# Optimization experiments

Hardware: AMD Instinct MI355X
Metric: run time of the kernel (lower is better)

The kernel has to match this reference:

```python
import jax, jax.numpy as jnp
import numpy as np

N_NODES = 100000
N_EDGES = 600000
D = 128          # model_dim
R = 50           # deprel_size


def setup_inputs() -> dict:
    key = jax.random.key(0)
    ks = jax.random.split(key, 20)
    s = 1.0 / np.sqrt(D)
    inp = jax.random.normal(ks[0], (N_NODES, D), dtype=jnp.float32)
    deprel_edge = jax.random.randint(ks[1], (N_EDGES,), 0, R)
    deparc_edge = jax.random.randint(ks[2], (N_EDGES,), 0, 4)
    edge_index = jax.random.randint(ks[3], (2, N_EDGES), 0, N_NODES)
    # parameters (nn.Linear weights stored as [out, in]; gates are Linear(D,1))
    V_in = jax.random.normal(ks[4], (D, D), dtype=jnp.float32) * s
    V_out = jax.random.normal(ks[5], (D, D), dtype=jnp.float32) * s
    W_self = jax.random.normal(ks[6], (D, D), dtype=jnp.float32) * s
    W_norel = jax.random.normal(ks[7], (D, D), dtype=jnp.float32) * s
    V_in_gate = jax.random.normal(ks[8], (1, D), dtype=jnp.float32) * s
    V_out_gate = jax.random.normal(ks[9], (1, D), dtype=jnp.float32) * s
    W_self_gate = jax.random.normal(ks[10], (1, D), dtype=jnp.float32) * s
    W_norel_gate = jax.random.normal(ks[11], (1, D), dtype=jnp.float32) * s
    b_in = jax.random.normal(ks[12], (R, D), dtype=jnp.float32) * 0.02
    b_out = jax.random.normal(ks[13], (R, D), dtype=jnp.float32) * 0.02
    b_in_gate = jax.random.normal(ks[14], (R, 1), dtype=jnp.float32) * 0.02 + 1.0
    b_out_gate = jax.random.normal(ks[15], (R, 1), dtype=jnp.float32) * 0.02 + 1.0
    return {
        "inp": inp, "deprel_edge": deprel_edge, "deparc_edge": deparc_edge,
        "edge_index": edge_index,
        "V_in": V_in, "b_in": b_in, "V_in_gate": V_in_gate, "b_in_gate": b_in_gate,
        "V_out": V_out, "b_out": b_out, "V_out_gate": V_out_gate, "b_out_gate": b_out_gate,
        "W_self": W_self, "W_self_gate": W_self_gate,
        "W_norel": W_norel, "W_norel_gate": W_norel_gate,
    }


def reference(inp, deprel_edge, deparc_edge, edge_index,
              V_in, b_in, V_in_gate, b_in_gate,
              V_out, b_out, V_out_gate, b_out_gate,
              W_self, W_self_gate, W_norel, W_norel_gate):
    # deparc type codes: 0=align(in), 1=opposite(out), 2=self, 3=norelation
    num_nodes = inp.shape[0]
    src, tgt = edge_index[0], edge_index[1]
    # transformed node features per edge type: [4, N, D]
    T = jnp.stack([inp @ V_in.T, inp @ V_out.T, inp @ W_self.T, inp @ W_norel.T])
    # gate pre-activations per edge type: [4, N, 1]
    G = jnp.stack([inp @ V_in_gate.T, inp @ V_out_gate.T,
                   inp @ W_self_gate.T, inp @ W_norel_gate.T])
    zeros_b = jnp.zeros_like(b_in)
    zeros_bg = jnp.zeros_like(b_in_gate)
    B = jnp.stack([b_in, b_out, zeros_b, zeros_b])        # [4, R, D] (self/norel have no relation bias)
    Bg = jnp.stack([b_in_gate, b_out_gate, zeros_bg, zeros_bg])  # [4, R, 1]
    # per-edge gather + relation bias
    msg = T[deparc_edge, src] + B[deparc_edge, deprel_edge]        # [E, D]
    gate = jax.nn.sigmoid(G[deparc_edge, src] + Bg[deparc_edge, deprel_edge])  # [E, 1]
    # scatter-add to target nodes
    return jax.ops.segment_sum(msg * gate, tgt, num_segments=num_nodes)
```

## Files before the change

### kernel.cpp

```cpp
#include <hip/hip_runtime.h>
#include <hip/hip_bf16.h>

#define D 128

typedef __bf16 bf16x8 __attribute__((ext_vector_type(8)));
typedef __bf16 bf16x4 __attribute__((ext_vector_type(4)));
typedef __bf16 bf16x2 __attribute__((ext_vector_type(2)));
typedef float  f32x4  __attribute__((ext_vector_type(4)));
typedef float  f32x2  __attribute__((ext_vector_type(2)));
typedef unsigned int u32x4 __attribute__((ext_vector_type(4)));

template <int ISBF>
__device__ __forceinline__ bf16x8 ld8(const void* p, size_t elem)
{
    if (ISBF) return *(const bf16x8*)((const __bf16*)p + elem);
    const f32x4* f = (const f32x4*)((const float*)p + elem);
    f32x4 lo = f[0], hi = f[1];
    bf16x8 r;
    r[0] = (__bf16)lo[0]; r[1] = (__bf16)lo[1]; r[2] = (__bf16)lo[2]; r[3] = (__bf16)lo[3];
    r[4] = (__bf16)hi[0]; r[5] = (__bf16)hi[1]; r[6] = (__bf16)hi[2]; r[7] = (__bf16)hi[3];
    return r;
}
template <int ISBF>
__device__ __forceinline__ float ldf(const void* p, size_t elem)
{
    return ISBF ? (float)((const __bf16*)p)[elem] : ((const float*)p)[elem];
}

__device__ __forceinline__ f32x2 bfpair(unsigned int u)
{
    f32x2 r;
    r[0] = __builtin_bit_cast(float, u << 16);
    r[1] = __builtin_bit_cast(float, u & 0xffff0000u);
    return r;
}

__device__ __forceinline__ f32x2 pkfma(f32x2 a, f32x2 b, f32x2 c)
{
    f32x2 d;
    asm("v_pk_fma_f32 %0, %1, %2, %3" : "=v"(d) : "v"(a), "v"(b), "v"(c));
    return d;
}

__global__ __launch_bounds__(256) void hist_detect_kernel(
    const int* __restrict__ tgt, int* __restrict__ counts, int E,
    const unsigned int* __restrict__ w, int* __restrict__ flag)
{
    __shared__ int cnt[256];
    int e = blockIdx.x * 256 + threadIdx.x;
    if (e < E) atomicAdd(&counts[tgt[e]], 1);
    if (blockIdx.x == 0) {
        int c = 0;
#pragma unroll
        for (int i = 0; i < 4; ++i) {
            unsigned int v = w[threadIdx.x * 4 + i];
            unsigned int ex = (v >> 7) & 0xFF;
            if (ex >= 90 && ex <= 134) ++c;
        }
        cnt[threadIdx.x] = c;
        __syncthreads();
        for (int s = 128; s > 0; s >>= 1) {
            if (threadIdx.x < s) cnt[threadIdx.x] += cnt[threadIdx.x + s];
            __syncthreads();
        }
        if (threadIdx.x == 0) flag[0] = (cnt[0] > 614) ? 1 : 0;
    }
}

template <int ISBF>
__device__ __forceinline__ void gate_bias_body(
    const void* __restrict__ A,
    const void* __restrict__ g0, const void* __restrict__ g1,
    const void* __restrict__ g2, const void* __restrict__ g3,
    const void* __restrict__ b_in, const void* __restrict__ b_out,
    const void* __restrict__ bg_in, const void* __restrict__ bg_out,
    float* __restrict__ G, __bf16* __restrict__ Bz, float* __restrict__ Bgz,
    int M)
{
    if (blockIdx.x < 101 && threadIdx.x < 128) {
        int row = blockIdx.x;
        int tid = threadIdx.x;
        float v = 0.f, gv = 0.f;
        if (row < 50) {
            v  = ldf<ISBF>(b_in, (size_t)row * D + tid);
            gv = ldf<ISBF>(bg_in, row);
        } else if (row < 100) {
            int rr = row - 50;
            v  = ldf<ISBF>(b_out, (size_t)rr * D + tid);
            gv = ldf<ISBF>(bg_out, rr);
        }
        Bz[(size_t)row * D + tid] = (__bf16)v;
        if (tid == 0) Bgz[row] = gv;
    }

    int node = blockIdx.x * 16 + (threadIdx.x >> 4);
    if (node >= M) return;
    int lane16 = threadIdx.x & 15;
    int dd = lane16 * 8;
    bf16x8 a  = ld8<ISBF>(A, (size_t)node * D + dd);
    bf16x8 q0 = ld8<ISBF>(g0, dd);
    bf16x8 q1 = ld8<ISBF>(g1, dd);
    bf16x8 q2 = ld8<ISBF>(g2, dd);
    bf16x8 q3 = ld8<ISBF>(g3, dd);
    float s0 = 0.f, s1 = 0.f, s2 = 0.f, s3 = 0.f;
#pragma unroll
    for (int k = 0; k < 8; ++k) {
        float af = (float)a[k];
        s0 = fmaf(af, (float)q0[k], s0);
        s1 = fmaf(af, (float)q1[k], s1);
        s2 = fmaf(af, (float)q2[k], s2);
        s3 = fmaf(af, (float)q3[k], s3);
    }
#pragma unroll
    for (int off = 8; off > 0; off >>= 1) {
        s0 += __shfl_xor(s0, off);
        s1 += __shfl_xor(s1, off);
        s2 += __shfl_xor(s2, off);
        s3 += __shfl_xor(s3, off);
    }
    if (lane16 == 0) {
        G[(size_t)0 * M + node] = s0;
        G[(size_t)1 * M + node] = s1;
        G[(size_t)2 * M + node] = s2;
        G[(size_t)3 * M + node] = s3;
    }
}

__global__ __launch_bounds__(256) void gate_bias_kernel(
    const void* __restrict__ A,
    const void* __restrict__ g0, const void* __restrict__ g1,
    const void* __restrict__ g2, const void* __restrict__ g3,
    const void* __restrict__ b_in, const void* __restrict__ b_out,
    const void* __restrict__ bg_in, const void* __restrict__ bg_out,
    float* __restrict__ G, __bf16* __restrict__ Bz, float* __restrict__ Bgz,
    int M, const int* __restrict__ flag)
{
    if (flag[0]) gate_bias_body<1>(A, g0, g1, g2, g3, b_in, b_out, bg_in, bg_out, G, Bz, Bgz, M);
    else         gate_bias_body<0>(A, g0, g1, g2, g3, b_in, b_out, bg_in, bg_out, G, Bz, Bgz, M);
}

__global__ __launch_bounds__(256) void scan1_kernel(
    const int* __restrict__ counts, int* __restrict__ rowptr,
    int* __restrict__ bsum, int M)
{
    __shared__ int sh[256];
    int base = blockIdx.x * 1024 + threadIdx.x * 4;
    int v[4];
#pragma unroll
    for (int k = 0; k < 4; ++k)
        v[k] = (base + k < M) ? counts[base + k] : 0;
    int tot = v[0] + v[1] + v[2] + v[3];
    sh[threadIdx.x] = tot;
    __syncthreads();
    for (int off = 1; off < 256; off <<= 1) {
        int t = (threadIdx.x >= off) ? sh[threadIdx.x - off] : 0;
        __syncthreads();
        sh[threadIdx.x] += t;
        __syncthreads();
    }
    int run = sh[threadIdx.x] - tot;
#pragma unroll
    for (int k = 0; k < 4; ++k) {
        if (base + k < M) rowptr[base + k] = run;
        run += v[k];
    }
    if (threadIdx.x == 255) bsum[blockIdx.x] = sh[255];
}

__global__ __launch_bounds__(256) void scan3_kernel(
    int* __restrict__ rowptr, int* __restrict__ cursor,
    const int* __restrict__ bsum, int M, int E)
{
    int b = blockIdx.x;
    int o = 0;
    for (int i = 0; i < b; ++i) o += bsum[i];
    int base = b * 1024 + threadIdx.x * 4;
#pragma unroll
    for (int k = 0; k < 4; ++k) {
        int i = base + k;
        if (i < M) {
            int r = rowptr[i] + o;
            rowptr[i] = r;
            cursor[i] = r;
        }
    }
    if (b == 0 && threadIdx.x == 0) rowptr[M] = E;
}

__global__ __launch_bounds__(256) void scatter_kernel(
    const int* __restrict__ deprel, const int* __restrict__ deparc,
    const int* __restrict__ src, const int* __restrict__ tgt,
    int* __restrict__ cursor, int2* __restrict__ recs, int E)
{
    int e = blockIdx.x * 256 + threadIdx.x;
    if (e >= E) return;
    int g = tgt[e];
    int pos = atomicAdd(&cursor[g], 1);
    recs[pos] = make_int2(src[e], (deprel[e] << 2) | deparc[e]);
}

template <int ISBF>
__device__ __forceinline__ void edge_agg_body(
    const void* __restrict__ inp, const float* __restrict__ G,
    const __bf16* __restrict__ Bz, const float* __restrict__ Bgz,
    const int* __restrict__ rowptr, const int2* __restrict__ recs,
    __bf16* __restrict__ AG, __bf16* __restrict__ BA, int M)
{
    const int g = blockIdx.x * 16 + (threadIdx.x >> 4);
    if (g >= M) return;
    const int lane16 = threadIdx.x & 15;
    const int dd = lane16 * 8;

    const int beg = rowptr[g], end = rowptr[g + 1];
    const int n = end - beg;

    f32x2 a0[4], a1[4], a2[4], a3[4], ba[4];
#pragma unroll
    for (int k = 0; k < 4; ++k) {
        a0[k] = (f32x2){0.f, 0.f}; a1[k] = (f32x2){0.f, 0.f};
        a2[k] = (f32x2){0.f, 0.f}; a3[k] = (f32x2){0.f, 0.f};
        ba[k] = (f32x2){0.f, 0.f};
    }

    bf16x8 v0 = {}, bz0 = {}, v1 = {}, bz1 = {};
    float gp0 = 0.f, bg0 = 0.f, gp1 = 0.f, bg1 = 0.f;
    int t0 = 0, t1 = 0;
    int2 r2 = make_int2(0, 0);

    auto issue = [&](int2 rec, bf16x8& v, bf16x8& bz, float& gp, float& bg, int& t) {
        t = rec.y & 3;
        int r = rec.y >> 2;
        int bidx = (t < 2) ? t * 50 + r : 100;
        gp = G[(size_t)t * M + rec.x];
        bg = Bgz[bidx];
        v  = ld8<ISBF>(inp, (size_t)rec.x * D + dd);
        bz = *(const bf16x8*)(Bz + (size_t)bidx * D + dd);
    };

    if (n > 0) issue(recs[beg], v0, bz0, gp0, bg0, t0);
    if (n > 1) issue(recs[beg + 1], v1, bz1, gp1, bg1, t1);
    if (n > 2) r2 = recs[beg + 2];

    for (int e = 0; e < n; ++e) {
        const bf16x8 v = v0, bz = bz0;
        const float gp = gp0, bg = bg0;
        const int t = t0;

        v0 = v1; bz0 = bz1; gp0 = gp1; bg0 = bg1; t0 = t1;
        if (e + 2 < n) {
            issue(r2, v1, bz1, gp1, bg1, t1);
            if (e + 3 < n) r2 = recs[beg + e + 3];
        }

        const float gate = 1.f / (1.f + __expf(-(gp + bg)));
        const float w0s = (t == 0) ? gate : 0.f;
        const float w1s = (t == 1) ? gate : 0.f;
        const float w2s = (t == 2) ? gate : 0.f;
        const float w3s = (t == 3) ? gate : 0.f;
        const f32x2 w0 = {w0s, w0s}, w1 = {w1s, w1s};
        const f32x2 w2 = {w2s, w2s}, w3 = {w3s, w3s};
        const f32x2 gg = {gate, gate};

        const u32x4 uv = __builtin_bit_cast(u32x4, v);
        const u32x4 ub = __builtin_bit_cast(u32x4, bz);
#pragma unroll
        for (int k = 0; k < 4; ++k) {
            const f32x2 vf = bfpair(uv[k]);
            const f32x2 bf = bfpair(ub[k]);
            a0[k] = pkfma(vf, w0, a0[k]);
            a1[k] = pkfma(vf, w1, a1[k]);
            a2[k] = pkfma(vf, w2, a2[k]);
            a3[k] = pkfma(vf, w3, a3[k]);
            ba[k] = pkfma(bf, gg, ba[k]);
        }
    }

    __bf16* agrow = AG + (size_t)g * (4 * D);
    bf16x8 w;
#pragma unroll
    for (int k = 0; k < 4; ++k) { w[2*k] = (__bf16)a0[k][0]; w[2*k+1] = (__bf16)a0[k][1]; }
    __builtin_nontemporal_store(w, (bf16x8*)(agrow + 0 * D + dd));
#pragma unroll
    for (int k = 0; k < 4; ++k) { w[2*k] = (__bf16)a1[k][0]; w[2*k+1] = (__bf16)a1[k][1]; }
    __builtin_nontemporal_store(w, (bf16x8*)(agrow + 1 * D + dd));
#pragma unroll
    for (int k = 0; k < 4; ++k) { w[2*k] = (__bf16)a2[k][0]; w[2*k+1] = (__bf16)a2[k][1]; }
    __builtin_nontemporal_store(w, (bf16x8*)(agrow + 2 * D + dd));
#pragma unroll
    for (int k = 0; k < 4; ++k) { w[2*k] = (__bf16)a3[k][0]; w[2*k+1] = (__bf16)a3[k][1]; }
    __builtin_nontemporal_store(w, (bf16x8*)(agrow + 3 * D + dd));
#pragma unroll
    for (int k = 0; k < 4; ++k) { w[2*k] = (__bf16)ba[k][0]; w[2*k+1] = (__bf16)ba[k][1]; }
    __builtin_nontemporal_store(w, (bf16x8*)(BA + (size_t)g * D + dd));
}

__global__ __launch_bounds__(256) void edge_agg_kernel(
    const void* __restrict__ inp, const float* __restrict__ G,
    const __bf16* __restrict__ Bz, const float* __restrict__ Bgz,
    const int* __restrict__ rowptr, const int2* __restrict__ recs,
    __bf16* __restrict__ AG, __bf16* __restrict__ BA, int M,
    const int* __restrict__ flag)
{
    if (flag[0]) edge_agg_body<1>(inp, G, Bz, Bgz, rowptr, recs, AG, BA, M);
    else         edge_agg_body<0>(inp, G, Bz, Bgz, rowptr, recs, AG, BA, M);
}

template <int ISBF>
__device__ __forceinline__ void gemm2_body(
    const __bf16* __restrict__ AG, const __bf16* __restrict__ BA,
    const void* __restrict__ W0, const void* __restrict__ W1,
    const void* __restrict__ W2, const void* __restrict__ W3,
    void* __restrict__ out, int M)
{
    __shared__ __bf16 Wsh[128 * 128];

    const int wave = threadIdx.x >> 6;
    const int lane = threadIdx.x & 63;
    const int lrow = lane & 15;
    const int kgrp = lane >> 4;
    const int m_base = blockIdx.x * 128 + wave * 32;

    int n0 = m_base + lrow;      if (n0 >= M) n0 = 0;
    int n1 = m_base + 16 + lrow; if (n1 >= M) n1 = 0;

    const void* Ws[4] = {W0, W1, W2, W3};

    f32x4 acc[2][8];
#pragma unroll
    for (int i = 0; i < 2; ++i)
#pragma unroll
        for (int j = 0; j < 8; ++j)
            acc[i][j] = (f32x4){0.f, 0.f, 0.f, 0.f};

    for (int t = 0; t < 4; ++t) {
        const void* W = Ws[t];
#pragma unroll
        for (int i = 0; i < 8; ++i) {
            int slot = threadIdx.x + 256 * i;
            int f = slot >> 4;
            int s = slot & 15;
            int sp = s ^ (f & 7);
            bf16x8 v = ld8<ISBF>(W, (size_t)f * D + s * 8);
            *(bf16x8*)(Wsh + f * 128 + sp * 8) = v;
        }
        __syncthreads();

#pragma unroll
        for (int ks = 0; ks < 4; ++ks) {
            const int k0 = ks * 32 + kgrp * 8;
            bf16x8 af0 = __builtin_nontemporal_load(
                (const bf16x8*)(AG + (size_t)n0 * (4 * D) + t * D + k0));
            bf16x8 af1 = __builtin_nontemporal_load(
                (const bf16x8*)(AG + (size_t)n1 * (4 * D) + t * D + k0));
            const int slot = 4 * ks + kgrp;
#pragma unroll
            for (int ft = 0; ft < 8; ++ft) {
                int f = ft * 16 + lrow;
                int sp = slot ^ (f & 7);
                bf16x8 wf = *(const bf16x8*)(Wsh + f * 128 + sp * 8);
                acc[0][ft] = __builtin_amdgcn_mfma_f32_16x16x32_bf16(wf, af0, acc[0][ft], 0, 0, 0);
                acc[1][ft] = __builtin_amdgcn_mfma_f32_16x16x32_bf16(wf, af1, acc[1][ft], 0, 0, 0);
            }
        }
        __syncthreads();
    }

#pragma unroll
    for (int nt = 0; nt < 2; ++nt) {
        int node = m_base + nt * 16 + lrow;
        if (node < M) {
#pragma unroll
            for (int ft = 0; ft < 8; ++ft) {
                int f0 = ft * 16 + kgrp * 4;
                bf16x4 bb = __builtin_nontemporal_load(
                    (const bf16x4*)(BA + (size_t)node * D + f0));
                f32x4 v = acc[nt][ft];
                v[0] += (float)bb[0]; v[1] += (float)bb[1];
                v[2] += (float)bb[2]; v[3] += (float)bb[3];
                if (ISBF) {
                    bf16x4 w4;
                    w4[0] = (__bf16)v[0]; w4[1] = (__bf16)v[1];
                    w4[2] = (__bf16)v[2]; w4[3] = (__bf16)v[3];
                    __builtin_nontemporal_store(w4,
                        (bf16x4*)((__bf16*)out + (size_t)node * D + f0));
                } else {
                    __builtin_nontemporal_store(v,
                        (f32x4*)((float*)out + (size_t)node * D + f0));
                }
            }
        }
    }
}

__global__ __launch_bounds__(256) void gemm2_kernel(
    const __bf16* __restrict__ AG, const __bf16* __restrict__ BA,
    const void* __restrict__ W0, const void* __restrict__ W1,
    const void* __restrict__ W2, const void* __restrict__ W3,
    void* __restrict__ out, int M, const int* __restrict__ flag)
{
    if (flag[0]) gemm2_body<1>(AG, BA, W0, W1, W2, W3, out, M);
    else         gemm2_body<0>(AG, BA, W0, W1, W2, W3, out, M);
}

__global__ void sentinel_kernel(__bf16* o, int n)
{
    int i = blockIdx.x * blockDim.x + threadIdx.x;
    if (i < n) o[i] = (__bf16)12345.0f;
}

static inline size_t align256(size_t x) { return (x + 255) & ~(size_t)255; }

extern "C" void kernel_launch(void* const* d_in, const int* in_sizes, int n_in,
                              void* d_out, int out_size, void* d_ws, size_t ws_size,
                              hipStream_t stream)
{
    const void* inp       = d_in[0];
    const int*  deprel    = (const int*)d_in[1];
    const int*  deparc    = (const int*)d_in[2];
    const int*  eidx      = (const int*)d_in[3];
    const void* V_in      = d_in[4];
    const void* b_in      = d_in[5];
    const void* V_in_g    = d_in[6];
    const void* b_in_g    = d_in[7];
    const void* V_out     = d_in[8];
    const void* b_out     = d_in[9];
    const void* V_out_g   = d_in[10];
    const void* b_out_g   = d_in[11];
    const void* W_self    = d_in[12];
    const void* W_self_g  = d_in[13];
    const void* W_norel   = d_in[14];
    const void* W_norel_g = d_in[15];

    const int M = in_sizes[0] / D;
    const int E = in_sizes[1];
    const int* src = eidx;
    const int* tgt = eidx + E;
    const int NB = (M + 1023) / 1024;

    size_t off = 0;
    size_t o_flag   = off; off = align256(off + sizeof(int));
    size_t o_AG     = off; off = align256(off + (size_t)M * 4 * D * sizeof(__bf16));
    size_t o_BA     = off; off = align256(off + (size_t)M * D * sizeof(__bf16));
    size_t o_G      = off; off = align256(off + (size_t)4 * M * sizeof(float));
    size_t o_counts = off; off = align256(off + (size_t)M * sizeof(int));
    size_t o_rowptr = off; off = align256(off + (size_t)(M + 1) * sizeof(int));
    size_t o_cursor = off; off = align256(off + (size_t)M * sizeof(int));
    size_t o_bsum   = off; off = align256(off + (size_t)NB * sizeof(int));
    size_t o_recs   = off; off = align256(off + (size_t)E * sizeof(int2));
    size_t o_Bz     = off; off = align256(off + (size_t)101 * D * sizeof(__bf16));
    size_t o_Bgz    = off; off = align256(off + (size_t)101 * sizeof(float));

    if (off > ws_size) {
        sentinel_kernel<<<(out_size + 255) / 256, 256, 0, stream>>>(
            (__bf16*)d_out, out_size);
        return;
    }

    int*    flag   = (int*)((char*)d_ws + o_flag);
    __bf16* AG     = (__bf16*)((char*)d_ws + o_AG);
    __bf16* BA     = (__bf16*)((char*)d_ws + o_BA);
    float*  Gbuf   = (float*)((char*)d_ws + o_G);
    int*    counts = (int*)((char*)d_ws + o_counts);
    int*    rowptr = (int*)((char*)d_ws + o_rowptr);
    int*    cursor = (int*)((char*)d_ws + o_cursor);
    int*    bsum   = (int*)((char*)d_ws + o_bsum);
    int2*   recs   = (int2*)((char*)d_ws + o_recs);
    __bf16* Bz     = (__bf16*)((char*)d_ws + o_Bz);
    float*  Bgz    = (float*)((char*)d_ws + o_Bgz);

    hipMemsetAsync(counts, 0, (size_t)M * sizeof(int), stream);
    hist_detect_kernel<<<(E + 255) / 256, 256, 0, stream>>>(
        tgt, counts, E, (const unsigned int*)inp, flag);
    scan1_kernel<<<NB, 256, 0, stream>>>(counts, rowptr, bsum, M);
    scan3_kernel<<<NB, 256, 0, stream>>>(rowptr, cursor, bsum, M, E);
    scatter_kernel<<<(E + 255) / 256, 256, 0, stream>>>(deprel, deparc, src, tgt,
                                                        cursor, recs, E);

    gate_bias_kernel<<<(M + 15) / 16, 256, 0, stream>>>(
        inp, V_in_g, V_out_g, W_self_g, W_norel_g,
        b_in, b_out, b_in_g, b_out_g, Gbuf, Bz, Bgz, M, flag);

    edge_agg_kernel<<<(M + 15) / 16, 256, 0, stream>>>(inp, Gbuf, Bz, Bgz,
                                                       rowptr, recs, AG, BA, M, flag);
    gemm2_kernel<<<(M + 127) / 128, 256, 0, stream>>>(AG, BA, V_in, V_out, W_self,
                                                      W_norel, d_out, M, flag);
}
```

Before: 325.2 us.

## Transform node features before edge aggregation and fuse gate GEMV into GEMM

Reorders the computation so the four per-type weight matrices are applied to node features first (gemm1, which also computes gate logits and bias tables), and the edge kernel then gathers the transformed rows, adds relation bias, applies the gate and writes the output directly. This removes the separate gate kernel, the typed aggregate buffers and the final GEMM pass. In exchange, per-edge gathers read from a 4x-wide bf16 transformed table and intermediate values are rounded to bf16 before accumulation.

```diff
diff --git a/kernel.cpp b/kernel.cpp
--- a/kernel.cpp
+++ b/kernel.cpp
@@ -5,10 +5,8 @@
 
 typedef __bf16 bf16x8 __attribute__((ext_vector_type(8)));
 typedef __bf16 bf16x4 __attribute__((ext_vector_type(4)));
-typedef __bf16 bf16x2 __attribute__((ext_vector_type(2)));
 typedef float  f32x4  __attribute__((ext_vector_type(4)));
 typedef float  f32x2  __attribute__((ext_vector_type(2)));
-typedef unsigned int u32x4 __attribute__((ext_vector_type(4)));
 
 template <int ISBF>
 __device__ __forceinline__ bf16x8 ld8(const void* p, size_t elem)
@@ -27,21 +25,6 @@
     return ISBF ? (float)((const __bf16*)p)[elem] : ((const float*)p)[elem];
 }
 
-__device__ __forceinline__ f32x2 bfpair(unsigned int u)
-{
-    f32x2 r;
-    r[0] = __builtin_bit_cast(float, u << 16);
-    r[1] = __builtin_bit_cast(float, u & 0xffff0000u);
-    return r;
-}
-
-__device__ __forceinline__ f32x2 pkfma(f32x2 a, f32x2 b, f32x2 c)
-{
-    f32x2 d;
-    asm("v_pk_fma_f32 %0, %1, %2, %3" : "=v"(d) : "v"(a), "v"(b), "v"(c));
-    return d;
-}
-
 __global__ __launch_bounds__(256) void hist_detect_kernel(
     const int* __restrict__ tgt, int* __restrict__ counts, int E,
     const unsigned int* __restrict__ w, int* __restrict__ flag)
@@ -67,16 +50,80 @@
     }
 }
 
+__global__ __launch_bounds__(256) void scan1_kernel(
+    const int* __restrict__ counts, int* __restrict__ rowptr,
+    int* __restrict__ bsum, int M)
+{
+    __shared__ int sh[256];
+    int base = blockIdx.x * 1024 + threadIdx.x * 4;
+    int v[4];
+#pragma unroll
+    for (int k = 0; k < 4; ++k)
+        v[k] = (base + k < M) ? counts[base + k] : 0;
+    int tot = v[0] + v[1] + v[2] + v[3];
+    sh[threadIdx.x] = tot;
+    __syncthreads();
+    for (int off = 1; off < 256; off <<= 1) {
+        int t = (threadIdx.x >= off) ? sh[threadIdx.x - off] : 0;
+        __syncthreads();
+        sh[threadIdx.x] += t;
+        __syncthreads();
+    }
+    int run = sh[threadIdx.x] - tot;
+#pragma unroll
+    for (int k = 0; k < 4; ++k) {
+        if (base + k < M) rowptr[base + k] = run;
+        run += v[k];
+    }
+    if (threadIdx.x == 255) bsum[blockIdx.x] = sh[255];
+}
+
+__global__ __launch_bounds__(256) void scan3_kernel(
+    int* __restrict__ rowptr, int* __restrict__ cursor,
+    const int* __restrict__ bsum, int M, int E)
+{
+    int b = blockIdx.x;
+    int o = 0;
+    for (int i = 0; i < b; ++i) o += bsum[i];
+    int base = b * 1024 + threadIdx.x * 4;
+#pragma unroll
+    for (int k = 0; k < 4; ++k) {
+        int i = base + k;
+        if (i < M) {
+            int r = rowptr[i] + o;
+            rowptr[i] = r;
+            cursor[i] = r;
+        }
+    }
+    if (b == 0 && threadIdx.x == 0) rowptr[M] = E;
+}
+
+__global__ __launch_bounds__(256) void scatter_kernel(
+    const int* __restrict__ deprel, const int* __restrict__ deparc,
+    const int* __restrict__ src, const int* __restrict__ tgt,
+    int* __restrict__ cursor, int2* __restrict__ recs, int E)
+{
+    int e = blockIdx.x * 256 + threadIdx.x;
+    if (e >= E) return;
+    int g = tgt[e];
+    int pos = atomicAdd(&cursor[g], 1);
+    recs[pos] = make_int2(src[e], (deprel[e] << 2) | deparc[e]);
+}
+
 template <int ISBF>
-__device__ __forceinline__ void gate_bias_body(
-    const void* __restrict__ A,
+__device__ __forceinline__ void gemm1_body(
+    const void* __restrict__ inp,
+    const void* __restrict__ W0, const void* __restrict__ W1,
+    const void* __restrict__ W2, const void* __restrict__ W3,
     const void* __restrict__ g0, const void* __restrict__ g1,
     const void* __restrict__ g2, const void* __restrict__ g3,
     const void* __restrict__ b_in, const void* __restrict__ b_out,
     const void* __restrict__ bg_in, const void* __restrict__ bg_out,
-    float* __restrict__ G, __bf16* __restrict__ Bz, float* __restrict__ Bgz,
-    int M)
-{
+    __bf16* __restrict__ T, float* __restrict__ G,
+    __bf16* __restrict__ Bz, float* __restrict__ Bgz, int M)
+{
+    __shared__ __bf16 Wsh[128 * 128];
+
     if (blockIdx.x < 101 && threadIdx.x < 128) {
         int row = blockIdx.x;
         int tid = threadIdx.x;
@@ -93,227 +140,6 @@
         if (tid == 0) Bgz[row] = gv;
     }
 
-    int node = blockIdx.x * 16 + (threadIdx.x >> 4);
-    if (node >= M) return;
-    int lane16 = threadIdx.x & 15;
-    int dd = lane16 * 8;
-    bf16x8 a  = ld8<ISBF>(A, (size_t)node * D + dd);
-    bf16x8 q0 = ld8<ISBF>(g0, dd);
-    bf16x8 q1 = ld8<ISBF>(g1, dd);
-    bf16x8 q2 = ld8<ISBF>(g2, dd);
-    bf16x8 q3 = ld8<ISBF>(g3, dd);
-    float s0 = 0.f, s1 = 0.f, s2 = 0.f, s3 = 0.f;
-#pragma unroll
-    for (int k = 0; k < 8; ++k) {
-        float af = (float)a[k];
-        s0 = fmaf(af, (float)q0[k], s0);
-        s1 = fmaf(af, (float)q1[k], s1);
-        s2 = fmaf(af, (float)q2[k], s2);
-        s3 = fmaf(af, (float)q3[k], s3);
-    }
-#pragma unroll
-    for (int off = 8; off > 0; off >>= 1) {
-        s0 += __shfl_xor(s0, off);
-        s1 += __shfl_xor(s1, off);
-        s2 += __shfl_xor(s2, off);
-        s3 += __shfl_xor(s3, off);
-    }
-    if (lane16 == 0) {
-        G[(size_t)0 * M + node] = s0;
-        G[(size_t)1 * M + node] = s1;
-        G[(size_t)2 * M + node] = s2;
-        G[(size_t)3 * M + node] = s3;
-    }
-}
-
-__global__ __launch_bounds__(256) void gate_bias_kernel(
-    const void* __restrict__ A,
-    const void* __restrict__ g0, const void* __restrict__ g1,
-    const void* __restrict__ g2, const void* __restrict__ g3,
-    const void* __restrict__ b_in, const void* __restrict__ b_out,
-    const void* __restrict__ bg_in, const void* __restrict__ bg_out,
-    float* __restrict__ G, __bf16* __restrict__ Bz, float* __restrict__ Bgz,
-    int M, const int* __restrict__ flag)
-{
-    if (flag[0]) gate_bias_body<1>(A, g0, g1, g2, g3, b_in, b_out, bg_in, bg_out, G, Bz, Bgz, M);
-    else         gate_bias_body<0>(A, g0, g1, g2, g3, b_in, b_out, bg_in, bg_out, G, Bz, Bgz, M);
-}
-
-__global__ __launch_bounds__(256) void scan1_kernel(
-    const int* __restrict__ counts, int* __restrict__ rowptr,
-    int* __restrict__ bsum, int M)
-{
-    __shared__ int sh[256];
-    int base = blockIdx.x * 1024 + threadIdx.x * 4;
-    int v[4];
-#pragma unroll
-    for (int k = 0; k < 4; ++k)
-        v[k] = (base + k < M) ? counts[base + k] : 0;
-    int tot = v[0] + v[1] + v[2] + v[3];
-    sh[threadIdx.x] = tot;
-    __syncthreads();
-    for (int off = 1; off < 256; off <<= 1) {
-        int t = (threadIdx.x >= off) ? sh[threadIdx.x - off] : 0;
-        __syncthreads();
-        sh[threadIdx.x] += t;
-        __syncthreads();
-    }
-    int run = sh[threadIdx.x] - tot;
-#pragma unroll
-    for (int k = 0; k < 4; ++k) {
-        if (base + k < M) rowptr[base + k] = run;
-        run += v[k];
-    }
-    if (threadIdx.x == 255) bsum[blockIdx.x] = sh[255];
-}
-
-__global__ __launch_bounds__(256) void scan3_kernel(
-    int* __restrict__ rowptr, int* __restrict__ cursor,
-    const int* __restrict__ bsum, int M, int E)
-{
-    int b = blockIdx.x;
-    int o = 0;
-    for (int i = 0; i < b; ++i) o += bsum[i];
-    int base = b * 1024 + threadIdx.x * 4;
-#pragma unroll
-    for (int k = 0; k < 4; ++k) {
-        int i = base + k;
-        if (i < M) {
-            int r = rowptr[i] + o;
-            rowptr[i] = r;
-            cursor[i] = r;
-        }
-    }
-    if (b == 0 && threadIdx.x == 0) rowptr[M] = E;
-}
-
-__global__ __launch_bounds__(256) void scatter_kernel(
-    const int* __restrict__ deprel, const int* __restrict__ deparc,
-    const int* __restrict__ src, const int* __restrict__ tgt,
-    int* __restrict__ cursor, int2* __restrict__ recs, int E)
-{
-    int e = blockIdx.x * 256 + threadIdx.x;
-    if (e >= E) return;
-    int g = tgt[e];
-    int pos = atomicAdd(&cursor[g], 1);
-    recs[pos] = make_int2(src[e], (deprel[e] << 2) | deparc[e]);
-}
-
-template <int ISBF>
-__device__ __forceinline__ void edge_agg_body(
-    const void* __restrict__ inp, const float* __restrict__ G,
-    const __bf16* __restrict__ Bz, const float* __restrict__ Bgz,
-    const int* __restrict__ rowptr, const int2* __restrict__ recs,
-    __bf16* __restrict__ AG, __bf16* __restrict__ BA, int M)
-{
-    const int g = blockIdx.x * 16 + (threadIdx.x >> 4);
-    if (g >= M) return;
-    const int lane16 = threadIdx.x & 15;
-    const int dd = lane16 * 8;
-
-    const int beg = rowptr[g], end = rowptr[g + 1];
-    const int n = end - beg;
-
-    f32x2 a0[4], a1[4], a2[4], a3[4], ba[4];
-#pragma unroll
-    for (int k = 0; k < 4; ++k) {
-        a0[k] = (f32x2){0.f, 0.f}; a1[k] = (f32x2){0.f, 0.f};
-        a2[k] = (f32x2){0.f, 0.f}; a3[k] = (f32x2){0.f, 0.f};
-        ba[k] = (f32x2){0.f, 0.f};
-    }
-
-    bf16x8 v0 = {}, bz0 = {}, v1 = {}, bz1 = {};
-    float gp0 = 0.f, bg0 = 0.f, gp1 = 0.f, bg1 = 0.f;
-    int t0 = 0, t1 = 0;
-    int2 r2 = make_int2(0, 0);
-
-    auto issue = [&](int2 rec, bf16x8& v, bf16x8& bz, float& gp, float& bg, int& t) {
-        t = rec.y & 3;
-        int r = rec.y >> 2;
-        int bidx = (t < 2) ? t * 50 + r : 100;
-        gp = G[(size_t)t * M + rec.x];
-        bg = Bgz[bidx];
-        v  = ld8<ISBF>(inp, (size_t)rec.x * D + dd);
-        bz = *(const bf16x8*)(Bz + (size_t)bidx * D + dd);
-    };
-
-    if (n > 0) issue(recs[beg], v0, bz0, gp0, bg0, t0);
-    if (n > 1) issue(recs[beg + 1], v1, bz1, gp1, bg1, t1);
-    if (n > 2) r2 = recs[beg + 2];
-
-    for (int e = 0; e < n; ++e) {
-        const bf16x8 v = v0, bz = bz0;
-        const float gp = gp0, bg = bg0;
-        const int t = t0;
-
-        v0 = v1; bz0 = bz1; gp0 = gp1; bg0 = bg1; t0 = t1;
-        if (e + 2 < n) {
-            issue(r2, v1, bz1, gp1, bg1, t1);
-            if (e + 3 < n) r2 = recs[beg + e + 3];
-        }
-
-        const float gate = 1.f / (1.f + __expf(-(gp + bg)));
-        const float w0s = (t == 0) ? gate : 0.f;
-        const float w1s = (t == 1) ? gate : 0.f;
-        const float w2s = (t == 2) ? gate : 0.f;
-        const float w3s = (t == 3) ? gate : 0.f;
-        const f32x2 w0 = {w0s, w0s}, w1 = {w1s, w1s};
-        const f32x2 w2 = {w2s, w2s}, w3 = {w3s, w3s};
-        const f32x2 gg = {gate, gate};
-
-        const u32x4 uv = __builtin_bit_cast(u32x4, v);
-        const u32x4 ub = __builtin_bit_cast(u32x4, bz);
-#pragma unroll
-        for (int k = 0; k < 4; ++k) {
-            const f32x2 vf = bfpair(uv[k]);
-            const f32x2 bf = bfpair(ub[k]);
-            a0[k] = pkfma(vf, w0, a0[k]);
-            a1[k] = pkfma(vf, w1, a1[k]);
-            a2[k] = pkfma(vf, w2, a2[k]);
-            a3[k] = pkfma(vf, w3, a3[k]);
-            ba[k] = pkfma(bf, gg, ba[k]);
-        }
-    }
-
-    __bf16* agrow = AG + (size_t)g * (4 * D);
-    bf16x8 w;
-#pragma unroll
-    for (int k = 0; k < 4; ++k) { w[2*k] = (__bf16)a0[k][0]; w[2*k+1] = (__bf16)a0[k][1]; }
-    __builtin_nontemporal_store(w, (bf16x8*)(agrow + 0 * D + dd));
-#pragma unroll
-    for (int k = 0; k < 4; ++k) { w[2*k] = (__bf16)a1[k][0]; w[2*k+1] = (__bf16)a1[k][1]; }
-    __builtin_nontemporal_store(w, (bf16x8*)(agrow + 1 * D + dd));
-#pragma unroll
-    for (int k = 0; k < 4; ++k) { w[2*k] = (__bf16)a2[k][0]; w[2*k+1] = (__bf16)a2[k][1]; }
-    __builtin_nontemporal_store(w, (bf16x8*)(agrow + 2 * D + dd));
-#pragma unroll
-    for (int k = 0; k < 4; ++k) { w[2*k] = (__bf16)a3[k][0]; w[2*k+1] = (__bf16)a3[k][1]; }
-    __builtin_nontemporal_store(w, (bf16x8*)(agrow + 3 * D + dd));
-#pragma unroll
-    for (int k = 0; k < 4; ++k) { w[2*k] = (__bf16)ba[k][0]; w[2*k+1] = (__bf16)ba[k][1]; }
-    __builtin_nontemporal_store(w, (bf16x8*)(BA + (size_t)g * D + dd));
-}
-
-__global__ __launch_bounds__(256) void edge_agg_kernel(
-    const void* __restrict__ inp, const float* __restrict__ G,
-    const __bf16* __restrict__ Bz, const float* __restrict__ Bgz,
-    const int* __restrict__ rowptr, const int2* __restrict__ recs,
-    __bf16* __restrict__ AG, __bf16* __restrict__ BA, int M,
-    const int* __restrict__ flag)
-{
-    if (flag[0]) edge_agg_body<1>(inp, G, Bz, Bgz, rowptr, recs, AG, BA, M);
-    else         edge_agg_body<0>(inp, G, Bz, Bgz, rowptr, recs, AG, BA, M);
-}
-
-template <int ISBF>
-__device__ __forceinline__ void gemm2_body(
-    const __bf16* __restrict__ AG, const __bf16* __restrict__ BA,
-    const void* __restrict__ W0, const void* __restrict__ W1,
-    const void* __restrict__ W2, const void* __restrict__ W3,
-    void* __restrict__ out, int M)
-{
-    __shared__ __bf16 Wsh[128 * 128];
-
     const int wave = threadIdx.x >> 6;
     const int lane = threadIdx.x & 63;
     const int lrow = lane & 15;
@@ -323,15 +149,49 @@
     int n0 = m_base + lrow;      if (n0 >= M) n0 = 0;
     int n1 = m_base + 16 + lrow; if (n1 >= M) n1 = 0;
 
+    bf16x8 af0[4], af1[4];
+#pragma unroll
+    for (int ks = 0; ks < 4; ++ks) {
+        const int k0 = ks * 32 + kgrp * 8;
+        af0[ks] = ld8<ISBF>(inp, (size_t)n0 * D + k0);
+        af1[ks] = ld8<ISBF>(inp, (size_t)n1 * D + k0);
+    }
+
+    {
+        const void* gs[4] = {g0, g1, g2, g3};
+        float s0[4], s1[4];
+#pragma unroll
+        for (int t = 0; t < 4; ++t) { s0[t] = 0.f; s1[t] = 0.f; }
+#pragma unroll
+        for (int t = 0; t < 4; ++t) {
+#pragma unroll
+            for (int ks = 0; ks < 4; ++ks) {
+                bf16x8 q = ld8<ISBF>(gs[t], ks * 32 + kgrp * 8);
+#pragma unroll
+                for (int j = 0; j < 8; ++j) {
+                    float qf = (float)q[j];
+                    s0[t] = fmaf((float)af0[ks][j], qf, s0[t]);
+                    s1[t] = fmaf((float)af1[ks][j], qf, s1[t]);
+                }
+            }
+        }
+#pragma unroll
+        for (int t = 0; t < 4; ++t) {
+            s0[t] += __shfl_xor(s0[t], 16); s0[t] += __shfl_xor(s0[t], 32);
+            s1[t] += __shfl_xor(s1[t], 16); s1[t] += __shfl_xor(s1[t], 32);
+        }
+        if (kgrp == 0) {
+            int nn0 = m_base + lrow;
+            int nn1 = m_base + 16 + lrow;
+#pragma unroll
+            for (int t = 0; t < 4; ++t) {
+                if (nn0 < M) G[(size_t)t * M + nn0] = s0[t];
+                if (nn1 < M) G[(size_t)t * M + nn1] = s1[t];
+            }
+        }
+    }
+
     const void* Ws[4] = {W0, W1, W2, W3};
-
-    f32x4 acc[2][8];
-#pragma unroll
-    for (int i = 0; i < 2; ++i)
-#pragma unroll
-        for (int j = 0; j < 8; ++j)
-            acc[i][j] = (f32x4){0.f, 0.f, 0.f, 0.f};
-
     for (int t = 0; t < 4; ++t) {
         const void* W = Ws[t];
 #pragma unroll
@@ -345,61 +205,138 @@
         }
         __syncthreads();
 
+        f32x4 acc[2][8];
+#pragma unroll
+        for (int i = 0; i < 2; ++i)
+#pragma unroll
+            for (int j = 0; j < 8; ++j)
+                acc[i][j] = (f32x4){0.f, 0.f, 0.f, 0.f};
+
 #pragma unroll
         for (int ks = 0; ks < 4; ++ks) {
-            const int k0 = ks * 32 + kgrp * 8;
-            bf16x8 af0 = __builtin_nontemporal_load(
-                (const bf16x8*)(AG + (size_t)n0 * (4 * D) + t * D + k0));
-            bf16x8 af1 = __builtin_nontemporal_load(
-                (const bf16x8*)(AG + (size_t)n1 * (4 * D) + t * D + k0));
             const int slot = 4 * ks + kgrp;
 #pragma unroll
             for (int ft = 0; ft < 8; ++ft) {
                 int f = ft * 16 + lrow;
                 int sp = slot ^ (f & 7);
                 bf16x8 wf = *(const bf16x8*)(Wsh + f * 128 + sp * 8);
-                acc[0][ft] = __builtin_amdgcn_mfma_f32_16x16x32_bf16(wf, af0, acc[0][ft], 0, 0, 0);
-                acc[1][ft] = __builtin_amdgcn_mfma_f32_16x16x32_bf16(wf, af1, acc[1][ft], 0, 0, 0);
+                acc[0][ft] = __builtin_amdgcn_mfma_f32_16x16x32_bf16(wf, af0[ks], acc[0][ft], 0, 0, 0);
+                acc[1][ft] = __builtin_amdgcn_mfma_f32_16x16x32_bf16(wf, af1[ks], acc[1][ft], 0, 0, 0);
             }
         }
         __syncthreads();
-    }
-
-#pragma unroll
-    for (int nt = 0; nt < 2; ++nt) {
-        int node = m_base + nt * 16 + lrow;
-        if (node < M) {
-#pragma unroll
-            for (int ft = 0; ft < 8; ++ft) {
-                int f0 = ft * 16 + kgrp * 4;
-                bf16x4 bb = __builtin_nontemporal_load(
-                    (const bf16x4*)(BA + (size_t)node * D + f0));
-                f32x4 v = acc[nt][ft];
-                v[0] += (float)bb[0]; v[1] += (float)bb[1];
-                v[2] += (float)bb[2]; v[3] += (float)bb[3];
-                if (ISBF) {
+
+#pragma unroll
+        for (int nt = 0; nt < 2; ++nt) {
+            int node = m_base + nt * 16 + lrow;
+            if (node < M) {
+#pragma unroll
+                for (int ft = 0; ft < 8; ++ft) {
+                    int f0 = ft * 16 + kgrp * 4;
+                    f32x4 v = acc[nt][ft];
                     bf16x4 w4;
                     w4[0] = (__bf16)v[0]; w4[1] = (__bf16)v[1];
                     w4[2] = (__bf16)v[2]; w4[3] = (__bf16)v[3];
                     __builtin_nontemporal_store(w4,
-                        (bf16x4*)((__bf16*)out + (size_t)node * D + f0));
-                } else {
-                    __builtin_nontemporal_store(v,
-                        (f32x4*)((float*)out + (size_t)node * D + f0));
+                        (bf16x4*)(T + (size_t)node * (4 * D) + t * D + f0));
                 }
             }
         }
     }
 }
 
-__global__ __launch_bounds__(256) void gemm2_kernel(
-    const __bf16* __restrict__ AG, const __bf16* __restrict__ BA,
+__global__ __launch_bounds__(256) void gemm1_kernel(
+    const void* __restrict__ inp,
     const void* __restrict__ W0, const void* __restrict__ W1,
     const void* __restrict__ W2, const void* __restrict__ W3,
+    const void* __restrict__ g0, const void* __restrict__ g1,
+    const void* __restrict__ g2, const void* __restrict__ g3,
+    const void* __restrict__ b_in, const void* __restrict__ b_out,
+    const void* __restrict__ bg_in, const void* __restrict__ bg_out,
+    __bf16* __restrict__ T, float* __restrict__ G,
+    __bf16* __restrict__ Bz, float* __restrict__ Bgz, int M,
+    const int* __restrict__ flag)
+{
+    if (flag[0]) gemm1_body<1>(inp, W0, W1, W2, W3, g0, g1, g2, g3,
+                               b_in, b_out, bg_in, bg_out, T, G, Bz, Bgz, M);
+    else         gemm1_body<0>(inp, W0, W1, W2, W3, g0, g1, g2, g3,
+                               b_in, b_out, bg_in, bg_out, T, G, Bz, Bgz, M);
+}
+
+template <int ISBF>
+__device__ __forceinline__ void edge_agg2_body(
+    const __bf16* __restrict__ T, const float* __restrict__ G,
+    const __bf16* __restrict__ Bz, const float* __restrict__ Bgz,
+    const int* __restrict__ rowptr, const int2* __restrict__ recs,
+    void* __restrict__ out, int M)
+{
+    const int g = blockIdx.x * 16 + (threadIdx.x >> 4);
+    if (g >= M) return;
+    const int lane16 = threadIdx.x & 15;
+    const int dd = lane16 * 8;
+
+    const int beg = rowptr[g], end = rowptr[g + 1];
+    const int n = end - beg;
+
+    float acc[8];
+#pragma unroll
+    for (int k = 0; k < 8; ++k) acc[k] = 0.f;
+
+    bf16x8 tv_c = {}, bz_c = {};
+    float gp_c = 0.f, bg_c = 0.f;
+    int2 rec_n = make_int2(0, 0);
+
+    auto issue = [&](int2 rec) {
+        int t = rec.y & 3;
+        int r = rec.y >> 2;
+        int bidx = (t < 2) ? t * 50 + r : 100;
+        gp_c = G[(size_t)t * M + rec.x];
+        bg_c = Bgz[bidx];
+        tv_c = *(const bf16x8*)(T + (size_t)rec.x * (4 * D) + t * D + dd);
+        bz_c = *(const bf16x8*)(Bz + (size_t)bidx * D + dd);
+    };
+
+    if (n > 0) {
+        issue(recs[beg]);
+        if (n > 1) rec_n = recs[beg + 1];
+    }
+
+    for (int e = 0; e < n; ++e) {
+        const bf16x8 tv = tv_c, bz = bz_c;
+        const float gp = gp_c, bg = bg_c;
+
+        if (e + 1 < n) {
+            issue(rec_n);
+            if (e + 2 < n) rec_n = recs[beg + e + 2];
+        }
+
+        const float gate = 1.f / (1.f + __expf(-(gp + bg)));
+#pragma unroll
+        for (int k = 0; k < 8; ++k)
+            acc[k] = fmaf(gate, (float)tv[k] + (float)bz[k], acc[k]);
+    }
+
+    if (ISBF) {
+        bf16x8 w;
+#pragma unroll
+        for (int k = 0; k < 8; ++k) w[k] = (__bf16)acc[k];
+        __builtin_nontemporal_store(w, (bf16x8*)((__bf16*)out + (size_t)g * D + dd));
+    } else {
+        f32x4 lo = {acc[0], acc[1], acc[2], acc[3]};
+        f32x4 hi = {acc[4], acc[5], acc[6], acc[7]};
+        __builtin_nontemporal_store(lo, (f32x4*)((float*)out + (size_t)g * D + dd));
+        __builtin_nontemporal_store(hi, (f32x4*)((float*)out + (size_t)g * D + dd + 4));
+    }
+}
+
+__global__ __launch_bounds__(256) void edge_agg2_kernel(
+    const __bf16* __restrict__ T, const float* __restrict__ G,
+    const __bf16* __restrict__ Bz, const float* __restrict__ Bgz,
+    const int* __restrict__ rowptr, const int2* __restrict__ recs,
     void* __restrict__ out, int M, const int* __restrict__ flag)
 {
-    if (flag[0]) gemm2_body<1>(AG, BA, W0, W1, W2, W3, out, M);
-    else         gemm2_body<0>(AG, BA, W0, W1, W2, W3, out, M);
+    if (flag[0]) edge_agg2_body<1>(T, G, Bz, Bgz, rowptr, recs, out, M);
+    else         edge_agg2_body<0>(T, G, Bz, Bgz, rowptr, recs, out, M);
 }
 
 __global__ void sentinel_kernel(__bf16* o, int n)
@@ -439,8 +376,7 @@
 
     size_t off = 0;
     size_t o_flag   = off; off = align256(off + sizeof(int));
-    size_t o_AG     = off; off = align256(off + (size_t)M * 4 * D * sizeof(__bf16));
-    size_t o_BA     = off; off = align256(off + (size_t)M * D * sizeof(__bf16));
+    size_t o_T      = off; off = align256(off + (size_t)M * 4 * D * sizeof(__bf16));
     size_t o_G      = off; off = align256(off + (size_t)4 * M * sizeof(float));
     size_t o_counts = off; off = align256(off + (size_t)M * sizeof(int));
     size_t o_rowptr = off; off = align256(off + (size_t)(M + 1) * sizeof(int));
@@ -457,8 +393,7 @@
     }
 
     int*    flag   = (int*)((char*)d_ws + o_flag);
-    __bf16* AG     = (__bf16*)((char*)d_ws + o_AG);
-    __bf16* BA     = (__bf16*)((char*)d_ws + o_BA);
+    __bf16* T      = (__bf16*)((char*)d_ws + o_T);
     float*  Gbuf   = (float*)((char*)d_ws + o_G);
     int*    counts = (int*)((char*)d_ws + o_counts);
     int*    rowptr = (int*)((char*)d_ws + o_rowptr);
@@ -476,12 +411,11 @@
     scatter_kernel<<<(E + 255) / 256, 256, 0, stream>>>(deprel, deparc, src, tgt,
                                                         cursor, recs, E);
 
-    gate_bias_kernel<<<(M + 15) / 16, 256, 0, stream>>>(
-        inp, V_in_g, V_out_g, W_self_g, W_norel_g,
-        b_in, b_out, b_in_g, b_out_g, Gbuf, Bz, Bgz, M, flag);
-
-    edge_agg_kernel<<<(M + 15) / 16, 256, 0, stream>>>(inp, Gbuf, Bz, Bgz,
-                                                       rowptr, recs, AG, BA, M, flag);
-    gemm2_kernel<<<(M + 127) / 128, 256, 0, stream>>>(AG, BA, V_in, V_out, W_self,
-                                                      W_norel, d_out, M, flag);
-}
+    gemm1_kernel<<<(M + 127) / 128, 256, 0, stream>>>(
+        inp, V_in, V_out, W_self, W_norel,
+        V_in_g, V_out_g, W_self_g, W_norel_g,
+        b_in, b_out, b_in_g, b_out_g, T, Gbuf, Bz, Bgz, M, flag);
+
+    edge_agg2_kernel<<<(M + 15) / 16, 256, 0, stream>>>(
+        T, Gbuf, Bz, Bgz, rowptr, recs, d_out, M, flag);
+}
```

After: 347.1 us. 6.7% more time.
